# Performance work log

Hardware: AMD Instinct MI355X
Metric: run time of the kernel (lower is better)

## Reference

```python
import jax, jax.numpy as jnp
import numpy as np

C_M, C_Z, C_H = 256, 128, 32
S, N = 128, 384
EPS = 1e-5


def setup_inputs() -> dict:
    key = jax.random.key(0)
    ks = jax.random.split(key, 8)
    sc = 1.0 / np.sqrt(C_M)
    return {
        "msa": jax.random.normal(ks[0], (S, N, C_M), dtype=jnp.float32),
        "ln_g": jnp.ones((C_M,), dtype=jnp.float32),
        "ln_b": jnp.zeros((C_M,), dtype=jnp.float32),
        "Wl": jax.random.uniform(ks[1], (C_M, C_H), jnp.float32, -sc, sc),
        "bl": jax.random.uniform(ks[2], (C_H,), jnp.float32, -sc, sc),
        "Wr": jax.random.uniform(ks[3], (C_M, C_H), jnp.float32, -sc, sc),
        "br": jax.random.uniform(ks[4], (C_H,), jnp.float32, -sc, sc),
        "Wo": jax.random.uniform(ks[5], (C_H * C_H, C_Z), jnp.float32, -1.0 / C_H, 1.0 / C_H),
        "bo": jax.random.uniform(ks[6], (C_Z,), jnp.float32, -1.0 / C_H, 1.0 / C_H),
    }


def _layernorm(x, g, b):
    mu = jnp.mean(x, axis=-1, keepdims=True)
    var = jnp.mean(jnp.square(x - mu), axis=-1, keepdims=True)
    return (x - mu) * jax.lax.rsqrt(var + EPS) * g + b


def reference(msa, ln_g, ln_b, Wl, bl, Wr, br, Wo, bo):
    s = msa.shape[0]
    m = _layernorm(msa, ln_g, ln_b)          # [s, n, c_m]
    left = m @ Wl + bl                        # [s, n, c_h]
    right = m @ Wr + br                       # [s, n, c_h]
    outer = jnp.einsum('sic,sjd->ijcd', left, right) / s  # [n, n, c_h, c_h]
    outer = outer.reshape(outer.shape[0], outer.shape[1], -1)
    return outer @ Wo + bo                    # [n, n, c_z]
```

## Files before the change

### kernel.cpp

```cpp
#include <hip/hip_runtime.h>
#include <hip/hip_bf16.h>

#define CM 256
#define CZ 128
#define CH 32
#define SS 128
#define NN 384

typedef short bf16x8 __attribute__((ext_vector_type(8)));
typedef float f32x4 __attribute__((ext_vector_type(4)));
typedef unsigned short us4 __attribute__((ext_vector_type(4)));
typedef unsigned short us8 __attribute__((ext_vector_type(8)));

__device__ __forceinline__ unsigned short f2bf(float f) {
    __hip_bfloat16 h = __float2bfloat16(f);
    return __builtin_bit_cast(unsigned short, h);
}

__global__ void k0_wo_t(const float* __restrict__ Wo, unsigned short* __restrict__ WoT) {
    int n = blockIdx.x;
    for (int k = threadIdx.x; k < CH * CH; k += blockDim.x) {
        WoT[n * (CH * CH) + k] = f2bf(Wo[(size_t)k * CZ + n]);
    }
}

__global__ __launch_bounds__(512) void k1_ln_proj(
    const float* __restrict__ msa, const float* __restrict__ g, const float* __restrict__ bta,
    const float* __restrict__ Wl, const float* __restrict__ bl,
    const float* __restrict__ Wr, const float* __restrict__ br,
    unsigned short* __restrict__ Lt, unsigned short* __restrict__ Rt)
{
    __shared__ unsigned short A_lds[128 * 264];
    __shared__ unsigned short B_lds[64 * 264];

    const int i    = blockIdx.x;
    const int t    = threadIdx.x;
    const int wv   = t >> 6;
    const int lane = t & 63;
    const int lr   = lane & 15, lg = lane >> 4;

    const float4 gv = ((const float4*)g)[lane];
    const float4 bv = ((const float4*)bta)[lane];
#pragma unroll 4
    for (int r = 0; r < 16; r++) {
        int s = wv * 16 + r;
        float4 v = ((const float4*)(msa + ((size_t)s * NN + i) * CM))[lane];
        float sum = v.x + v.y + v.z + v.w;
        float sq  = v.x * v.x + v.y * v.y + v.z * v.z + v.w * v.w;
#pragma unroll
        for (int off = 32; off >= 1; off >>= 1) {
            sum += __shfl_xor(sum, off, 64);
            sq  += __shfl_xor(sq, off, 64);
        }
        float mu = sum * (1.f / CM);
        float rs = rsqrtf(sq * (1.f / CM) - mu * mu + 1e-5f);
        us4 pk;
        pk[0] = f2bf((v.x - mu) * rs * gv.x + bv.x);
        pk[1] = f2bf((v.y - mu) * rs * gv.y + bv.y);
        pk[2] = f2bf((v.z - mu) * rs * gv.z + bv.z);
        pk[3] = f2bf((v.w - mu) * rs * gv.w + bv.w);
        *(us4*)&A_lds[s * 264 + lane * 4] = pk;
    }
#pragma unroll 4
    for (int u = 0; u < 16; u++) {
        int e = u * 512 + t;
        int ch = e & 31, k = e >> 5;
        B_lds[ch * 264 + k]        = f2bf(Wl[e]);
        B_lds[(32 + ch) * 264 + k] = f2bf(Wr[e]);
    }
    __syncthreads();

    const int m0 = (wv >> 1) * 32;
    const int n0 = (wv & 1) * 32;
    f32x4 acc[2][2];
#pragma unroll
    for (int a = 0; a < 2; a++)
#pragma unroll
        for (int b = 0; b < 2; b++) acc[a][b] = (f32x4){0.f, 0.f, 0.f, 0.f};

#pragma unroll
    for (int ks = 0; ks < 8; ks++) {
        int ko = ks * 32 + lg * 8;
        bf16x8 a0 = *(const bf16x8*)&A_lds[(m0 + lr) * 264 + ko];
        bf16x8 a1 = *(const bf16x8*)&A_lds[(m0 + 16 + lr) * 264 + ko];
        bf16x8 b0 = *(const bf16x8*)&B_lds[(n0 + lr) * 264 + ko];
        bf16x8 b1 = *(const bf16x8*)&B_lds[(n0 + 16 + lr) * 264 + ko];
        acc[0][0] = __builtin_amdgcn_mfma_f32_16x16x32_bf16(a0, b0, acc[0][0], 0, 0, 0);
        acc[0][1] = __builtin_amdgcn_mfma_f32_16x16x32_bf16(a0, b1, acc[0][1], 0, 0, 0);
        acc[1][0] = __builtin_amdgcn_mfma_f32_16x16x32_bf16(a1, b0, acc[1][0], 0, 0, 0);
        acc[1][1] = __builtin_amdgcn_mfma_f32_16x16x32_bf16(a1, b1, acc[1][1], 0, 0, 0);
    }

    const bool isL = (n0 == 0);
    const float scale = isL ? 0.0078125f : 1.f;
#pragma unroll
    for (int mt = 0; mt < 2; mt++)
#pragma unroll
        for (int nt = 0; nt < 2; nt++) {
            int ch = (n0 + nt * 16 + lr) & 31;
            float bias = isL ? bl[ch] : br[ch];
            us4 pk;
#pragma unroll
            for (int rg = 0; rg < 4; rg++)
                pk[rg] = f2bf((acc[mt][nt][rg] + bias) * scale);
            unsigned short* dst = (isL ? Lt : Rt) + (size_t)(i * CH + ch) * SS + m0 + mt * 16 + lg * 4;
            *(us4*)dst = pk;
        }
}

#define TI 8
#define TJ 8
#define P1_B_OFF 69632
#define OH1_OFF  65536
#define WO_OFF   131072
#define K2_LDS   163840

__global__ __launch_bounds__(512, 2) void k2_fused(
    const unsigned short* __restrict__ Lt, const unsigned short* __restrict__ Rt,
    const unsigned short* __restrict__ WoT, const float* __restrict__ bo,
    float* __restrict__ out)
{
    extern __shared__ char smem[];
    unsigned short* A = (unsigned short*)(smem);
    unsigned short* B = (unsigned short*)(smem + P1_B_OFF);

    const int i0 = blockIdx.x * TI;
    const int j0 = blockIdx.y * TJ;
    const int t  = threadIdx.x;
    const int wv = t >> 6, lane = t & 63;
    const int lr = lane & 15, lg = lane >> 4;

    const unsigned short* gA = Lt + (size_t)i0 * CH * SS;
    const unsigned short* gB = Rt + (size_t)j0 * CH * SS;
#pragma unroll
    for (int it = 0; it < 8; it++) {
        int c  = it * 512 + t;
        int rw = c >> 4, kc = c & 15;
        *(us8*)(A + rw * 136 + kc * 8) = *(const us8*)(gA + rw * 128 + kc * 8);
        *(us8*)(B + rw * 136 + kc * 8) = *(const us8*)(gB + rw * 128 + kc * 8);
    }
    __syncthreads();

    const int m0 = (wv >> 2) * 128;
    const int n0w = (wv & 3) * 64;

    f32x4 accE[4][4], accO[4][4];
#pragma unroll
    for (int a = 0; a < 4; a++)
#pragma unroll
        for (int b = 0; b < 4; b++) {
            accE[a][b] = (f32x4){0.f, 0.f, 0.f, 0.f};
            accO[a][b] = (f32x4){0.f, 0.f, 0.f, 0.f};
        }

#pragma unroll
    for (int ks = 0; ks < 4; ks++) {
        int ko = ks * 32 + lg * 8;
        bf16x8 af[8], bfr[4];
#pragma unroll
        for (int mt = 0; mt < 8; mt++) af[mt]  = *(const bf16x8*)(A + (m0 + mt * 16 + lr) * 136 + ko);
#pragma unroll
        for (int nt = 0; nt < 4; nt++) bfr[nt] = *(const bf16x8*)(B + (n0w + nt * 16 + lr) * 136 + ko);
#pragma unroll
        for (int mt = 0; mt < 8; mt++)
#pragma unroll
            for (int nt = 0; nt < 4; nt++) {
                if (mt & 1)
                    accO[mt >> 1][nt] = __builtin_amdgcn_mfma_f32_16x16x32_bf16(af[mt], bfr[nt], accO[mt >> 1][nt], 0, 0, 0);
                else
                    accE[mt >> 1][nt] = __builtin_amdgcn_mfma_f32_16x16x32_bf16(af[mt], bfr[nt], accE[mt >> 1][nt], 0, 0, 0);
            }
    }
    __syncthreads();

    {
        unsigned short* Oh0 = (unsigned short*)smem;
        unsigned short* Oh1 = (unsigned short*)(smem + OH1_OFF);
#pragma unroll
        for (int mh = 0; mh < 4; mh++) {
            int iiw = (wv >> 2) * 4 + mh;
#pragma unroll
            for (int nt = 0; nt < 4; nt++)
#pragma unroll
                for (int rg = 0; rg < 4; rg++) {
                    int rowH = iiw * 16 + lg * 4 + rg;
                    int col  = n0w + nt * 16 + lr;
                    int okey = ((rowH >> 5) ^ (rowH >> 2)) & 7;
                    int chk  = (col >> 3) ^ okey;
                    Oh0[rowH * 256 + chk * 8 + (col & 7)] = f2bf(accE[mh][nt][rg]);
                    Oh1[rowH * 256 + chk * 8 + (col & 7)] = f2bf(accO[mh][nt][rg]);
                }
        }
    }

    const int zsl = wv & 1, ksl = wv >> 1;
    unsigned short* WB = (unsigned short*)(smem + WO_OFF);

    f32x4 acc2[4][4];
#pragma unroll
    for (int a = 0; a < 4; a++)
#pragma unroll
        for (int b = 0; b < 4; b++) acc2[a][b] = (f32x4){0.f, 0.f, 0.f, 0.f};

    for (int c = 0; c < 8; c++) {
        __syncthreads();
        {
#pragma unroll
            for (int q = 0; q < 4; q++) {
                int lam = q * 512 + t;
                int z = lam >> 4, cc = lam & 15;
                int cg = cc ^ (z & 15);
                *(us8*)&WB[lam * 8] = *(const us8*)&WoT[(size_t)z * 1024 + c * 128 + cg * 8];
            }
        }
        __syncthreads();

        const int cch = c * 4 + ksl;
        const int hh  = cch >> 4;
        const int cH  = cch & 15;
        const unsigned short* OhX = (const unsigned short*)(smem + (hh ? OH1_OFF : 0));

        bf16x8 af2[4], bf2[4];
#pragma unroll
        for (int ai = 0; ai < 4; ai++) {
            int rowH = (ai * 2 + ((lane >> 3) & 1)) * 16 + cH;
            int okey = ((rowH >> 5) ^ (rowH >> 2)) & 7;
            int chk  = (((lane & 7) * 4 + lg) ^ okey);
            af2[ai] = *(const bf16x8*)&OhX[rowH * 256 + chk * 8];
        }
#pragma unroll
        for (int bi = 0; bi < 4; bi++) {
            int z = zsl * 64 + bi * 16 + lr;
            int chk = (ksl * 4 + lg) ^ (z & 15);
            bf2[bi] = *(const bf16x8*)&WB[z * 128 + chk * 8];
        }
#pragma unroll
        for (int ai = 0; ai < 4; ai++)
#pragma unroll
            for (int bi = 0; bi < 4; bi++)
                acc2[ai][bi] = __builtin_amdgcn_mfma_f32_16x16x32_bf16(af2[ai], bf2[bi], acc2[ai][bi], 0, 0, 0);
    }
    __syncthreads();

    float* RB = (float*)smem;
#pragma unroll
    for (int ai = 0; ai < 4; ai++)
#pragma unroll
        for (int bi = 0; bi < 4; bi++) {
            int z  = zsl * 64 + bi * 16 + lr;
            int pr = ai * 16 + lg * 4;
            *(f32x4*)&RB[ksl * 8704 + z * 68 + pr] = acc2[ai][bi];
        }
    __syncthreads();

    {
        int z = t >> 2, pq = t & 3;
        float bz = bo[z];
#pragma unroll
        for (int u = 0; u < 4; u++) {
            int p0r = pq * 16 + u * 4;
            f32x4 s = (f32x4){0.f, 0.f, 0.f, 0.f};
#pragma unroll
            for (int ks2 = 0; ks2 < 4; ks2++)
                s += *(const f32x4*)&RB[ks2 * 8704 + z * 68 + p0r];
#pragma unroll
            for (int e = 0; e < 4; e++) {
                int p = p0r + e;
                out[((size_t)(i0 + (p >> 3)) * NN + (j0 + (p & 7))) * CZ + z] = s[e] + bz;
            }
        }
    }
}

extern "C" void kernel_launch(void* const* d_in, const int* in_sizes, int n_in,
                              void* d_out, int out_size, void* d_ws, size_t ws_size,
                              hipStream_t stream) {
    const float* msa  = (const float*)d_in[0];
    const float* ln_g = (const float*)d_in[1];
    const float* ln_b = (const float*)d_in[2];
    const float* Wl   = (const float*)d_in[3];
    const float* bl   = (const float*)d_in[4];
    const float* Wr   = (const float*)d_in[5];
    const float* br   = (const float*)d_in[6];
    const float* Wo   = (const float*)d_in[7];
    const float* bo   = (const float*)d_in[8];
    float* out = (float*)d_out;

    unsigned short* Lt  = (unsigned short*)d_ws;
    unsigned short* Rt  = Lt + (size_t)NN * CH * SS;
    unsigned short* WoT = Rt + (size_t)NN * CH * SS;

    hipFuncSetAttribute((const void*)k2_fused,
                        hipFuncAttributeMaxDynamicSharedMemorySize, K2_LDS);

    k0_wo_t<<<dim3(CZ), dim3(256), 0, stream>>>(Wo, WoT);
    k1_ln_proj<<<dim3(NN), dim3(512), 0, stream>>>(msa, ln_g, ln_b, Wl, bl, Wr, br, Lt, Rt);
    k2_fused<<<dim3(NN / TI, NN / TJ), dim3(512), K2_LDS, stream>>>(Lt, Rt, WoT, bo, out);
}
```

Baseline: 248.8 us.

## Split LN-projection over S halves, pre-transpose Wl/Wr, prefetch Wo chunks into registers

The Wl/Wr bf16 transposes move into the k0 kernel, so k1 loads pre-converted weights with vector copies. k1 now runs as two 256-thread blocks per residue, each covering half of the S rows, which doubles the block count. In k2 the MFMA operands are swapped so each lane holds four consecutive columns; the outer-product staging then writes packed us4 values with a new swizzle instead of scalar stores. The next Wo chunk is also prefetched into registers, overlapping its global load with the current chunk's MFMAs at the cost of extra registers.

```diff
diff --git a/kernel.cpp b/kernel.cpp
--- a/kernel.cpp
+++ b/kernel.cpp
@@ -17,23 +17,31 @@
     return __builtin_bit_cast(unsigned short, h);
 }
 
-__global__ void k0_wo_t(const float* __restrict__ Wo, unsigned short* __restrict__ WoT) {
+__global__ __launch_bounds__(256) void k0_transpose(
+    const float* __restrict__ Wo, const float* __restrict__ Wl, const float* __restrict__ Wr,
+    unsigned short* __restrict__ WoT, unsigned short* __restrict__ WT) {
     int n = blockIdx.x;
     for (int k = threadIdx.x; k < CH * CH; k += blockDim.x) {
         WoT[n * (CH * CH) + k] = f2bf(Wo[(size_t)k * CZ + n]);
     }
-}
-
-__global__ __launch_bounds__(512) void k1_ln_proj(
+    int k = threadIdx.x;
+    if (n < 32) {
+        WT[n * CM + k] = f2bf(Wl[(size_t)k * CH + n]);
+    } else if (n < 64) {
+        WT[32 * CM + (n - 32) * CM + k] = f2bf(Wr[(size_t)k * CH + (n - 32)]);
+    }
+}
+
+__global__ __launch_bounds__(256, 2) void k1_ln_proj(
     const float* __restrict__ msa, const float* __restrict__ g, const float* __restrict__ bta,
-    const float* __restrict__ Wl, const float* __restrict__ bl,
-    const float* __restrict__ Wr, const float* __restrict__ br,
+    const unsigned short* __restrict__ WT, const float* __restrict__ bl, const float* __restrict__ br,
     unsigned short* __restrict__ Lt, unsigned short* __restrict__ Rt)
 {
-    __shared__ unsigned short A_lds[128 * 264];
+    __shared__ unsigned short A_lds[64 * 264];
     __shared__ unsigned short B_lds[64 * 264];
 
     const int i    = blockIdx.x;
+    const int sh   = blockIdx.y;
     const int t    = threadIdx.x;
     const int wv   = t >> 6;
     const int lane = t & 63;
@@ -43,7 +51,8 @@
     const float4 bv = ((const float4*)bta)[lane];
 #pragma unroll 4
     for (int r = 0; r < 16; r++) {
-        int s = wv * 16 + r;
+        int sl = wv * 16 + r;
+        int s  = sh * 64 + sl;
         float4 v = ((const float4*)(msa + ((size_t)s * NN + i) * CM))[lane];
         float sum = v.x + v.y + v.z + v.w;
         float sq  = v.x * v.x + v.y * v.y + v.z * v.z + v.w * v.w;
@@ -59,14 +68,12 @@
         pk[1] = f2bf((v.y - mu) * rs * gv.y + bv.y);
         pk[2] = f2bf((v.z - mu) * rs * gv.z + bv.z);
         pk[3] = f2bf((v.w - mu) * rs * gv.w + bv.w);
-        *(us4*)&A_lds[s * 264 + lane * 4] = pk;
-    }
-#pragma unroll 4
-    for (int u = 0; u < 16; u++) {
-        int e = u * 512 + t;
-        int ch = e & 31, k = e >> 5;
-        B_lds[ch * 264 + k]        = f2bf(Wl[e]);
-        B_lds[(32 + ch) * 264 + k] = f2bf(Wr[e]);
+        *(us4*)&A_lds[sl * 264 + lane * 4] = pk;
+    }
+#pragma unroll
+    for (int u = 0; u < 8; u++) {
+        int id = u * 256 + t;
+        *(us8*)&B_lds[(id >> 5) * 264 + (id & 31) * 8] = *(const us8*)&WT[id * 8];
     }
     __syncthreads();
 
@@ -103,7 +110,8 @@
 #pragma unroll
             for (int rg = 0; rg < 4; rg++)
                 pk[rg] = f2bf((acc[mt][nt][rg] + bias) * scale);
-            unsigned short* dst = (isL ? Lt : Rt) + (size_t)(i * CH + ch) * SS + m0 + mt * 16 + lg * 4;
+            unsigned short* dst = (isL ? Lt : Rt) + (size_t)(i * CH + ch) * SS
+                                  + sh * 64 + m0 + mt * 16 + lg * 4;
             *(us4*)dst = pk;
         }
 }
@@ -141,7 +149,7 @@
     }
     __syncthreads();
 
-    const int m0 = (wv >> 2) * 128;
+    const int m0  = (wv >> 2) * 128;
     const int n0w = (wv & 3) * 64;
 
     f32x4 accE[4][4], accO[4][4];
@@ -166,30 +174,44 @@
 #pragma unroll
             for (int nt = 0; nt < 4; nt++) {
                 if (mt & 1)
-                    accO[mt >> 1][nt] = __builtin_amdgcn_mfma_f32_16x16x32_bf16(af[mt], bfr[nt], accO[mt >> 1][nt], 0, 0, 0);
+                    accO[mt >> 1][nt] = __builtin_amdgcn_mfma_f32_16x16x32_bf16(bfr[nt], af[mt], accO[mt >> 1][nt], 0, 0, 0);
                 else
-                    accE[mt >> 1][nt] = __builtin_amdgcn_mfma_f32_16x16x32_bf16(af[mt], bfr[nt], accE[mt >> 1][nt], 0, 0, 0);
+                    accE[mt >> 1][nt] = __builtin_amdgcn_mfma_f32_16x16x32_bf16(bfr[nt], af[mt], accE[mt >> 1][nt], 0, 0, 0);
             }
     }
     __syncthreads();
+
+    us8 wreg[4];
+#pragma unroll
+    for (int q = 0; q < 4; q++) {
+        int lam = q * 512 + t;
+        int z = lam >> 4, cc = lam & 15;
+        int cg = cc ^ (z & 15);
+        wreg[q] = *(const us8*)&WoT[(size_t)z * 1024 + cg * 8];
+    }
 
     {
         unsigned short* Oh0 = (unsigned short*)smem;
         unsigned short* Oh1 = (unsigned short*)(smem + OH1_OFF);
 #pragma unroll
         for (int mh = 0; mh < 4; mh++) {
-            int iiw = (wv >> 2) * 4 + mh;
-#pragma unroll
-            for (int nt = 0; nt < 4; nt++)
+            int iiw  = (wv >> 2) * 4 + mh;
+            int rowH = iiw * 16 + lr;
+            int okey = (rowH ^ (rowH >> 4)) & 7;
+#pragma unroll
+            for (int nt = 0; nt < 4; nt++) {
+                int colBase = n0w + nt * 16 + lg * 4;
+                int chk = (colBase >> 3) ^ okey;
+                int off = rowH * 256 + chk * 8 + (lg & 1) * 4;
+                us4 pkE, pkO;
 #pragma unroll
                 for (int rg = 0; rg < 4; rg++) {
-                    int rowH = iiw * 16 + lg * 4 + rg;
-                    int col  = n0w + nt * 16 + lr;
-                    int okey = ((rowH >> 5) ^ (rowH >> 2)) & 7;
-                    int chk  = (col >> 3) ^ okey;
-                    Oh0[rowH * 256 + chk * 8 + (col & 7)] = f2bf(accE[mh][nt][rg]);
-                    Oh1[rowH * 256 + chk * 8 + (col & 7)] = f2bf(accO[mh][nt][rg]);
+                    pkE[rg] = f2bf(accE[mh][nt][rg]);
+                    pkO[rg] = f2bf(accO[mh][nt][rg]);
                 }
+                *(us4*)&Oh0[off] = pkE;
+                *(us4*)&Oh1[off] = pkO;
+            }
         }
     }
 
@@ -204,13 +226,18 @@
 
     for (int c = 0; c < 8; c++) {
         __syncthreads();
-        {
+#pragma unroll
+        for (int q = 0; q < 4; q++) {
+            int lam = q * 512 + t;
+            *(us8*)&WB[lam * 8] = wreg[q];
+        }
+        if (c < 7) {
 #pragma unroll
             for (int q = 0; q < 4; q++) {
                 int lam = q * 512 + t;
                 int z = lam >> 4, cc = lam & 15;
                 int cg = cc ^ (z & 15);
-                *(us8*)&WB[lam * 8] = *(const us8*)&WoT[(size_t)z * 1024 + c * 128 + cg * 8];
+                wreg[q] = *(const us8*)&WoT[(size_t)z * 1024 + (c + 1) * 128 + cg * 8];
             }
         }
         __syncthreads();
@@ -224,7 +251,7 @@
 #pragma unroll
         for (int ai = 0; ai < 4; ai++) {
             int rowH = (ai * 2 + ((lane >> 3) & 1)) * 16 + cH;
-            int okey = ((rowH >> 5) ^ (rowH >> 2)) & 7;
+            int okey = (rowH ^ (rowH >> 4)) & 7;
             int chk  = (((lane & 7) * 4 + lg) ^ okey);
             af2[ai] = *(const bf16x8*)&OhX[rowH * 256 + chk * 8];
         }
@@ -289,11 +316,12 @@
     unsigned short* Lt  = (unsigned short*)d_ws;
     unsigned short* Rt  = Lt + (size_t)NN * CH * SS;
     unsigned short* WoT = Rt + (size_t)NN * CH * SS;
+    unsigned short* WT  = WoT + (size_t)CZ * CH * CH;
 
     hipFuncSetAttribute((const void*)k2_fused,
                         hipFuncAttributeMaxDynamicSharedMemorySize, K2_LDS);
 
-    k0_wo_t<<<dim3(CZ), dim3(256), 0, stream>>>(Wo, WoT);
-    k1_ln_proj<<<dim3(NN), dim3(512), 0, stream>>>(msa, ln_g, ln_b, Wl, bl, Wr, br, Lt, Rt);
+    k0_transpose<<<dim3(CZ), dim3(256), 0, stream>>>(Wo, Wl, Wr, WoT, WT);
+    k1_ln_proj<<<dim3(NN, 2), dim3(256), 0, stream>>>(msa, ln_g, ln_b, WT, bl, br, Lt, Rt);
     k2_fused<<<dim3(NN / TI, NN / TJ), dim3(512), K2_LDS, stream>>>(Lt, Rt, WoT, bo, out);
 }
```

Result: faster. 221.6 us (-10.9%).
